# Kernel optimization log

Measured on AMD Instinct MI355X. Metric: run time of the kernel, lower is better.

## Reference

```python
import jax, jax.numpy as jnp
import numpy as np

MARGIN = 0.3
POS_THRESH_M = 25.0
NEG_THRESH_M = 100.0
EARTH_R = 6371000.0
B, D = 1024, 256


def _pairwise_haversine(gps):
    # gps: [B,2] degrees -> [B,B] meters
    lat = jnp.deg2rad(gps[:, 0])
    dlat = jnp.deg2rad(gps[None, :, 0] - gps[:, None, 0])
    dlon = jnp.deg2rad(gps[None, :, 1] - gps[:, None, 1])
    a = jnp.sin(dlat / 2) ** 2 + jnp.cos(lat)[:, None] * jnp.cos(lat)[None, :] * jnp.sin(dlon / 2) ** 2
    return EARTH_R * 2.0 * jnp.arctan2(jnp.sqrt(a), jnp.sqrt(1.0 - a))


def _pairwise_euclidean(emb):
    # faithful to torch.norm(emb[None]-emb[:,None], dim=-1), with safe sqrt at 0
    diff = emb[None, :, :] - emb[:, None, :]          # [B,B,D]
    sq = jnp.sum(diff * diff, axis=-1)                # [B,B]
    return jnp.where(sq > 0, jnp.sqrt(jnp.where(sq > 0, sq, 1.0)), 0.0)


def setup_inputs() -> dict:
    key = jax.random.key(0)
    k1, k2 = jax.random.split(key)
    embeddings = jax.random.normal(k1, (B, D), dtype=jnp.float32)
    # small geographic box (~222 m x ~182 m) so both positive (<25 m) and
    # negative (>100 m) pairs exist for nearly every anchor
    base = jnp.array([35.0, 139.0], dtype=jnp.float32)
    gps_coords = base + jax.random.uniform(k2, (B, 2), dtype=jnp.float32) * 0.002
    return {"embeddings": embeddings, "gps_coords": gps_coords}


def reference(embeddings, gps_coords):
    n = embeddings.shape[0]
    gps_d = _pairwise_haversine(gps_coords)           # [B,B]
    emb_d = _pairwise_euclidean(embeddings)           # [B,B]
    eye = jnp.eye(n, dtype=bool)
    pos_mask = (gps_d < POS_THRESH_M) & ~eye
    neg_mask = gps_d > NEG_THRESH_M

    has_pos = jnp.any(pos_mask, axis=1)
    has_neg = jnp.any(neg_mask, axis=1)
    valid = has_pos & has_neg                         # anchors contributing a triplet

    # hardest positive per anchor (masked max)
    d_ap = jnp.max(jnp.where(pos_mask, emb_d, -1.0), axis=1)          # [B]

    # semi-hard negatives: d_ap < d < d_ap + margin among negatives
    semi_mask = neg_mask & (emb_d > d_ap[:, None]) & (emb_d < d_ap[:, None] + MARGIN)
    has_semi = jnp.any(semi_mask, axis=1)
    BIG = jnp.float32(1e9)
    semi_min = jnp.min(jnp.where(semi_mask, emb_d, BIG), axis=1)
    neg_min = jnp.min(jnp.where(neg_mask, emb_d, BIG), axis=1)        # fallback: hardest negative
    d_an = jnp.where(has_semi, semi_min, neg_min)

    triplet = jax.nn.relu(d_ap - d_an + MARGIN)
    triplet = jnp.where(valid, triplet, 0.0)
    n_triplets = jnp.sum(valid.astype(jnp.float32))
    loss = jnp.sum(triplet) / jnp.maximum(n_triplets, 1.0)
    return loss
```

## Files before the change

kernel.cpp:

```cpp
#include <hip/hip_runtime.h>
#include <hip/hip_bf16.h>

typedef __attribute__((ext_vector_type(8))) short bf16x8;
typedef __attribute__((ext_vector_type(4))) float f32x4;

#define NB 1024
#define ND 256
#define KC 512
#define MARGINF 0.3f
#define BIGV 1e9f
#define D2R 0.017453292519943295f
#define HD2R 0.008726646259971648f

#define A_POS 3.8495040e-12f
#define A_NEG 6.1592064e-11f

__device__ __forceinline__ float d4(float4 a, float4 b, float acc) {
    return fmaf(a.x,b.x, fmaf(a.y,b.y, fmaf(a.z,b.z, fmaf(a.w,b.w, acc))));
}

__global__ __launch_bounds__(256) void prep_kernel(
    const float* __restrict__ emb, const float* __restrict__ gps,
    float4* __restrict__ prep, unsigned short* __restrict__ C)
{
    const int tid = threadIdx.x;
    const int row = blockIdx.x*16 + (tid >> 4);
    const int kk  = tid & 15;
    const float4* r4 = (const float4*)emb + (size_t)row*64;
    float s = 0.f;
    #pragma unroll
    for (int c = 0; c < 4; ++c) {
        float4 v = r4[kk + 16*c];
        s = d4(v, v, s);
        float fv[4] = {v.x, v.y, v.z, v.w};
        unsigned short hh[4], ll[4];
        #pragma unroll
        for (int q = 0; q < 4; ++q) {
            __hip_bfloat16 hb = __float2bfloat16(fv[q]);
            float hf = __bfloat162float(hb);
            __hip_bfloat16 lb = __float2bfloat16(fv[q] - hf);
            hh[q] = *(unsigned short*)&hb;
            ll[q] = *(unsigned short*)&lb;
        }
        *(ushort4*)(C + (size_t)row*KC +       4*(kk+16*c)) = make_ushort4(hh[0],hh[1],hh[2],hh[3]);
        *(ushort4*)(C + (size_t)row*KC + 256 + 4*(kk+16*c)) = make_ushort4(ll[0],ll[1],ll[2],ll[3]);
    }
    #pragma unroll
    for (int off = 1; off < 16; off <<= 1) s += __shfl_xor(s, off);
    if (kk == 0) {
        float2 g = ((const float2*)gps)[row];
        prep[row] = make_float4(s, g.x, g.y, cosf(g.x * D2R));
    }
}

__global__ __launch_bounds__(256) void gram_mfma(
    const unsigned short* __restrict__ C, const float4* __restrict__ prep,
    float* __restrict__ sEnc, float* __restrict__ pP)
{
    __shared__ float sRed[64][33];

    const int tid = threadIdx.x, lane = tid & 63, w = tid >> 6;
    const int wr = w >> 1, wc = w & 1;
    const int ib = blockIdx.x & 15, jb = blockIdx.x >> 4;
    const int i0 = ib*64, j0 = jb*64;
    const int lr = lane & 15, lk = lane >> 4;
    const short* Cs = (const short*)C;

    f32x4 acc[2][2] = {};
    #pragma unroll 4
    for (int ks = 0; ks < 16; ++ks) {
        bf16x8 a0 = *(const bf16x8*)(Cs + (size_t)(i0 + wr*32      + lr)*KC + ks*32 + lk*8);
        bf16x8 a1 = *(const bf16x8*)(Cs + (size_t)(i0 + wr*32 + 16 + lr)*KC + ks*32 + lk*8);
        bf16x8 b0 = *(const bf16x8*)(Cs + (size_t)(j0 + wc*32      + lr)*KC + ks*32 + lk*8);
        bf16x8 b1 = *(const bf16x8*)(Cs + (size_t)(j0 + wc*32 + 16 + lr)*KC + ks*32 + lk*8);
        acc[0][0] = __builtin_amdgcn_mfma_f32_16x16x32_bf16(a0, b0, acc[0][0], 0, 0, 0);
        acc[0][1] = __builtin_amdgcn_mfma_f32_16x16x32_bf16(a0, b1, acc[0][1], 0, 0, 0);
        acc[1][0] = __builtin_amdgcn_mfma_f32_16x16x32_bf16(a1, b0, acc[1][0], 0, 0, 0);
        acc[1][1] = __builtin_amdgcn_mfma_f32_16x16x32_bf16(a1, b1, acc[1][1], 0, 0, 0);
    }

    float4 pj[2];
    pj[0] = prep[j0 + wc*32 + lr];
    pj[1] = prep[j0 + wc*32 + 16 + lr];

    #pragma unroll
    for (int fi = 0; fi < 2; ++fi) {
        #pragma unroll
        for (int r = 0; r < 4; ++r) {
            const int rl = wr*32 + fi*16 + lk*4 + r;
            const int gi = i0 + rl;
            const float4 pi = prep[gi];
            float pmax = -1.f;
            #pragma unroll
            for (int fj = 0; fj < 2; ++fj) {
                const int gj = j0 + wc*32 + fj*16 + lr;
                float d2v = pi.x + pj[fj].x - 2.f*acc[fi][fj][r];
                d2v = d2v > 0.f ? d2v : 0.f;
                const float sla = sinf((pj[fj].y - pi.y) * HD2R);
                const float slo = sinf((pj[fj].z - pi.z) * HD2R);
                const float hav = fmaf(sla, sla, (pi.w * pj[fj].w) * (slo*slo));
                const bool pos = (hav < A_POS) && (gi != gj);
                const bool neg = (hav > A_NEG);
                pmax = fmaxf(pmax, pos ? d2v : -1.f);
                sEnc[(size_t)gi*NB + gj] = neg ? d2v : BIGV;
            }
            sRed[rl][lr + 16*wc] = pmax;
        }
    }
    __syncthreads();
    if (tid < 64) {
        float m = sRed[tid][0];
        #pragma unroll
        for (int c = 1; c < 32; ++c) m = fmaxf(m, sRed[tid][c]);
        pP[(i0 + tid)*16 + jb] = m;
    }
}

__global__ __launch_bounds__(256) void rows_kernel(
    const float* __restrict__ sEnc, const float* __restrict__ pP,
    float* __restrict__ tri, float* __restrict__ val)
{
    const int tid = threadIdx.x, lane = tid & 63, w = tid >> 6;
    const int i = blockIdx.x*4 + w;

    float p = pP[i*16 + (lane & 15)];
    #pragma unroll
    for (int off = 1; off < 16; off <<= 1) p = fmaxf(p, __shfl_xor(p, off));
    const float dap2 = p;
    const bool has_pos = dap2 > -0.5f;
    float lo2 = -1.f, hi2 = -1.f;
    if (has_pos) { const float hb = sqrtf(dap2) + MARGINF; lo2 = dap2; hi2 = hb*hb; }

    float nmin = BIGV, smin = BIGV;
    const float4* __restrict__ row = (const float4*)sEnc + (size_t)i*256;
    #pragma unroll
    for (int pss = 0; pss < 4; ++pss) {
        const float4 x = row[pss*64 + lane];
        #pragma unroll
        for (int q = 0; q < 4; ++q) {
            const float xc = (q==0) ? x.x : (q==1) ? x.y : (q==2) ? x.z : x.w;
            nmin = fminf(nmin, xc);
            smin = fminf(smin, (xc > lo2 && xc < hi2) ? xc : BIGV);
        }
    }
    #pragma unroll
    for (int off = 1; off < 64; off <<= 1) {
        nmin = fminf(nmin, __shfl_xor(nmin, off));
        smin = fminf(smin, __shfl_xor(smin, off));
    }
    if (lane == 0) {
        const bool has_neg  = nmin < 0.5f*BIGV;
        const bool has_semi = smin < 0.5f*BIGV;
        const float dan2 = has_semi ? smin : nmin;
        const float dap  = has_pos ? sqrtf(dap2) : 0.f;
        float t = dap - sqrtf(dan2) + MARGINF;
        t = t > 0.f ? t : 0.f;
        const bool valid = has_pos && has_neg;
        tri[i] = valid ? t : 0.f;
        val[i] = valid ? 1.f : 0.f;
    }
}

__global__ __launch_bounds__(256) void finalize_kernel(
    const float* __restrict__ tri, const float* __restrict__ val, float* __restrict__ out)
{
    const int tid = threadIdx.x;
    float st = 0.f, sv = 0.f;
    #pragma unroll
    for (int g = 0; g < 4; ++g) { st += tri[tid + (g<<8)]; sv += val[tid + (g<<8)]; }
    #pragma unroll
    for (int off = 1; off < 64; off <<= 1) { st += __shfl_xor(st, off); sv += __shfl_xor(sv, off); }
    __shared__ float rt[4], rv[4];
    if ((tid & 63) == 0) { rt[tid>>6] = st; rv[tid>>6] = sv; }
    __syncthreads();
    if (tid == 0) {
        float t = rt[0]+rt[1]+rt[2]+rt[3];
        float v = rv[0]+rv[1]+rv[2]+rv[3];
        out[0] = t / fmaxf(v, 1.f);
    }
}

extern "C" void kernel_launch(void* const* d_in, const int* in_sizes, int n_in,
                              void* d_out, int out_size, void* d_ws, size_t ws_size,
                              hipStream_t stream) {
    const float* emb = (const float*)d_in[0];
    const float* gps = (const float*)d_in[1];
    float* ws = (float*)d_ws;

    float*          sEnc = ws;
    unsigned short* Cbf  = (unsigned short*)(ws + 1048576);
    float4*         prep = (float4*)(ws + 1048576 + 262144);
    float*          pP   = ws + 1048576 + 262144 + 4096;
    float*          tri  = pP + 16384;
    float*          val  = tri + 1024;

    prep_kernel<<<64, 256, 0, stream>>>(emb, gps, prep, Cbf);
    gram_mfma<<<256, 256, 0, stream>>>(Cbf, prep, sEnc, pP);
    rows_kernel<<<256, 256, 0, stream>>>(sEnc, pP, tri, val);
    finalize_kernel<<<1, 256, 0, stream>>>(tri, val, (float*)d_out);
}
```

Measured before the change: 28.58 us.

## Fuse prep kernel into gram MFMA with on-the-fly bf16 hi/lo split

Removes the separate prep kernel and computes row norms, gps cosines and the bf16 high/low split inside the gram kernel, with norms and gps staged in shared memory. The MFMA loop now does three products per k-chunk (HH, LH, HL), where the old code ran a single product over a concatenated hi|lo layout. This saves one launch and the round trip through the intermediate bf16 buffer. In exchange every block redoes the conversion and norm work for its tiles, reads fp32 rows directly, and issues more MFMAs.

Measured after the change: 27.42 us. -4.1%, faster.

```diff
diff --git a/kernel.cpp b/kernel.cpp
--- a/kernel.cpp
+++ b/kernel.cpp
@@ -6,7 +6,6 @@
 
 #define NB 1024
 #define ND 256
-#define KC 512
 #define MARGINF 0.3f
 #define BIGV 1e9f
 #define D2R 0.017453292519943295f
@@ -19,69 +18,82 @@
     return fmaf(a.x,b.x, fmaf(a.y,b.y, fmaf(a.z,b.z, fmaf(a.w,b.w, acc))));
 }
 
-__global__ __launch_bounds__(256) void prep_kernel(
+__device__ __forceinline__ void splitHL(float4 v0, float4 v1, bf16x8& H, bf16x8& L) {
+    float f[8] = {v0.x, v0.y, v0.z, v0.w, v1.x, v1.y, v1.z, v1.w};
+    #pragma unroll
+    for (int q = 0; q < 8; ++q) {
+        __hip_bfloat16 h = __float2bfloat16(f[q]);
+        float hf = __bfloat162float(h);
+        __hip_bfloat16 l = __float2bfloat16(f[q] - hf);
+        H[q] = *(short*)&h;
+        L[q] = *(short*)&l;
+    }
+}
+
+__global__ __launch_bounds__(256) void gram_mfma(
     const float* __restrict__ emb, const float* __restrict__ gps,
-    float4* __restrict__ prep, unsigned short* __restrict__ C)
-{
-    const int tid = threadIdx.x;
-    const int row = blockIdx.x*16 + (tid >> 4);
-    const int kk  = tid & 15;
-    const float4* r4 = (const float4*)emb + (size_t)row*64;
-    float s = 0.f;
-    #pragma unroll
-    for (int c = 0; c < 4; ++c) {
-        float4 v = r4[kk + 16*c];
-        s = d4(v, v, s);
-        float fv[4] = {v.x, v.y, v.z, v.w};
-        unsigned short hh[4], ll[4];
-        #pragma unroll
-        for (int q = 0; q < 4; ++q) {
-            __hip_bfloat16 hb = __float2bfloat16(fv[q]);
-            float hf = __bfloat162float(hb);
-            __hip_bfloat16 lb = __float2bfloat16(fv[q] - hf);
-            hh[q] = *(unsigned short*)&hb;
-            ll[q] = *(unsigned short*)&lb;
-        }
-        *(ushort4*)(C + (size_t)row*KC +       4*(kk+16*c)) = make_ushort4(hh[0],hh[1],hh[2],hh[3]);
-        *(ushort4*)(C + (size_t)row*KC + 256 + 4*(kk+16*c)) = make_ushort4(ll[0],ll[1],ll[2],ll[3]);
-    }
-    #pragma unroll
-    for (int off = 1; off < 16; off <<= 1) s += __shfl_xor(s, off);
-    if (kk == 0) {
-        float2 g = ((const float2*)gps)[row];
-        prep[row] = make_float4(s, g.x, g.y, cosf(g.x * D2R));
-    }
-}
-
-__global__ __launch_bounds__(256) void gram_mfma(
-    const unsigned short* __restrict__ C, const float4* __restrict__ prep,
     float* __restrict__ sEnc, float* __restrict__ pP)
 {
-    __shared__ float sRed[64][33];
+    __shared__ float  sSqI[64], sSqJ[64];
+    __shared__ float4 sGI[64], sGJ[64];
+    __shared__ float  sRed[64][33];
 
     const int tid = threadIdx.x, lane = tid & 63, w = tid >> 6;
     const int wr = w >> 1, wc = w & 1;
     const int ib = blockIdx.x & 15, jb = blockIdx.x >> 4;
     const int i0 = ib*64, j0 = jb*64;
     const int lr = lane & 15, lk = lane >> 4;
-    const short* Cs = (const short*)C;
+    const float4* __restrict__ emb4 = (const float4*)emb;
+
+    {
+        const int half = tid & 1, r = (tid >> 1) & 63;
+        const int base = (tid < 128) ? i0 : j0;
+        const float4* rp = emb4 + (size_t)(base + r)*64 + half*32;
+        float s = 0.f;
+        #pragma unroll
+        for (int q = 0; q < 32; ++q) s = d4(rp[q], rp[q], s);
+        s += __shfl_xor(s, 1);
+        if (half == 0) { if (tid < 128) sSqI[r] = s; else sSqJ[r] = s; }
+    }
+    if (tid < 128) {
+        const int r = tid & 63;
+        const int base = (tid < 64) ? i0 : j0;
+        float2 g = ((const float2*)gps)[base + r];
+        float4 gi = make_float4(g.x, g.y, cosf(g.x * D2R), 0.f);
+        if (tid < 64) sGI[r] = gi; else sGJ[r] = gi;
+    }
+    __syncthreads();
 
     f32x4 acc[2][2] = {};
-    #pragma unroll 4
-    for (int ks = 0; ks < 16; ++ks) {
-        bf16x8 a0 = *(const bf16x8*)(Cs + (size_t)(i0 + wr*32      + lr)*KC + ks*32 + lk*8);
-        bf16x8 a1 = *(const bf16x8*)(Cs + (size_t)(i0 + wr*32 + 16 + lr)*KC + ks*32 + lk*8);
-        bf16x8 b0 = *(const bf16x8*)(Cs + (size_t)(j0 + wc*32      + lr)*KC + ks*32 + lk*8);
-        bf16x8 b1 = *(const bf16x8*)(Cs + (size_t)(j0 + wc*32 + 16 + lr)*KC + ks*32 + lk*8);
-        acc[0][0] = __builtin_amdgcn_mfma_f32_16x16x32_bf16(a0, b0, acc[0][0], 0, 0, 0);
-        acc[0][1] = __builtin_amdgcn_mfma_f32_16x16x32_bf16(a0, b1, acc[0][1], 0, 0, 0);
-        acc[1][0] = __builtin_amdgcn_mfma_f32_16x16x32_bf16(a1, b0, acc[1][0], 0, 0, 0);
-        acc[1][1] = __builtin_amdgcn_mfma_f32_16x16x32_bf16(a1, b1, acc[1][1], 0, 0, 0);
-    }
-
-    float4 pj[2];
-    pj[0] = prep[j0 + wc*32 + lr];
-    pj[1] = prep[j0 + wc*32 + 16 + lr];
+    #pragma unroll 2
+    for (int k8 = 0; k8 < 8; ++k8) {
+        const int co = k8*8 + lk*2;
+        const float4* pa0 = emb4 + (size_t)(i0 + wr*32      + lr)*64 + co;
+        const float4* pa1 = emb4 + (size_t)(i0 + wr*32 + 16 + lr)*64 + co;
+        const float4* pb0 = emb4 + (size_t)(j0 + wc*32      + lr)*64 + co;
+        const float4* pb1 = emb4 + (size_t)(j0 + wc*32 + 16 + lr)*64 + co;
+        bf16x8 a0H,a0L,a1H,a1L,b0H,b0L,b1H,b1L;
+        splitHL(pa0[0], pa0[1], a0H, a0L);
+        splitHL(pa1[0], pa1[1], a1H, a1L);
+        splitHL(pb0[0], pb0[1], b0H, b0L);
+        splitHL(pb1[0], pb1[1], b1H, b1L);
+        acc[0][0] = __builtin_amdgcn_mfma_f32_16x16x32_bf16(a0H, b0H, acc[0][0], 0,0,0);
+        acc[0][1] = __builtin_amdgcn_mfma_f32_16x16x32_bf16(a0H, b1H, acc[0][1], 0,0,0);
+        acc[1][0] = __builtin_amdgcn_mfma_f32_16x16x32_bf16(a1H, b0H, acc[1][0], 0,0,0);
+        acc[1][1] = __builtin_amdgcn_mfma_f32_16x16x32_bf16(a1H, b1H, acc[1][1], 0,0,0);
+        acc[0][0] = __builtin_amdgcn_mfma_f32_16x16x32_bf16(a0L, b0H, acc[0][0], 0,0,0);
+        acc[0][1] = __builtin_amdgcn_mfma_f32_16x16x32_bf16(a0L, b1H, acc[0][1], 0,0,0);
+        acc[1][0] = __builtin_amdgcn_mfma_f32_16x16x32_bf16(a1L, b0H, acc[1][0], 0,0,0);
+        acc[1][1] = __builtin_amdgcn_mfma_f32_16x16x32_bf16(a1L, b1H, acc[1][1], 0,0,0);
+        acc[0][0] = __builtin_amdgcn_mfma_f32_16x16x32_bf16(a0H, b0L, acc[0][0], 0,0,0);
+        acc[0][1] = __builtin_amdgcn_mfma_f32_16x16x32_bf16(a0H, b1L, acc[0][1], 0,0,0);
+        acc[1][0] = __builtin_amdgcn_mfma_f32_16x16x32_bf16(a1H, b0L, acc[1][0], 0,0,0);
+        acc[1][1] = __builtin_amdgcn_mfma_f32_16x16x32_bf16(a1H, b1L, acc[1][1], 0,0,0);
+    }
+
+    float sqj[2]; float4 gj2[2];
+    sqj[0] = sSqJ[wc*32 + lr];      gj2[0] = sGJ[wc*32 + lr];
+    sqj[1] = sSqJ[wc*32 + 16 + lr]; gj2[1] = sGJ[wc*32 + 16 + lr];
 
     #pragma unroll
     for (int fi = 0; fi < 2; ++fi) {
@@ -89,16 +101,17 @@
         for (int r = 0; r < 4; ++r) {
             const int rl = wr*32 + fi*16 + lk*4 + r;
             const int gi = i0 + rl;
-            const float4 pi = prep[gi];
+            const float sqi = sSqI[rl];
+            const float4 gvi = sGI[rl];
             float pmax = -1.f;
             #pragma unroll
             for (int fj = 0; fj < 2; ++fj) {
                 const int gj = j0 + wc*32 + fj*16 + lr;
-                float d2v = pi.x + pj[fj].x - 2.f*acc[fi][fj][r];
+                float d2v = sqi + sqj[fj] - 2.f*acc[fi][fj][r];
                 d2v = d2v > 0.f ? d2v : 0.f;
-                const float sla = sinf((pj[fj].y - pi.y) * HD2R);
-                const float slo = sinf((pj[fj].z - pi.z) * HD2R);
-                const float hav = fmaf(sla, sla, (pi.w * pj[fj].w) * (slo*slo));
+                const float sla = sinf((gj2[fj].x - gvi.x) * HD2R);
+                const float slo = sinf((gj2[fj].y - gvi.y) * HD2R);
+                const float hav = fmaf(sla, sla, (gvi.z * gj2[fj].z) * (slo*slo));
                 const bool pos = (hav < A_POS) && (gi != gj);
                 const bool neg = (hav > A_NEG);
                 pmax = fmaxf(pmax, pos ? d2v : -1.f);
@@ -187,15 +200,12 @@
     const float* gps = (const float*)d_in[1];
     float* ws = (float*)d_ws;
 
-    float*          sEnc = ws;
-    unsigned short* Cbf  = (unsigned short*)(ws + 1048576);
-    float4*         prep = (float4*)(ws + 1048576 + 262144);
-    float*          pP   = ws + 1048576 + 262144 + 4096;
-    float*          tri  = pP + 16384;
-    float*          val  = tri + 1024;
-
-    prep_kernel<<<64, 256, 0, stream>>>(emb, gps, prep, Cbf);
-    gram_mfma<<<256, 256, 0, stream>>>(Cbf, prep, sEnc, pP);
+    float* sEnc = ws;
+    float* pP   = ws + 1048576;
+    float* tri  = pP + 16384;
+    float* val  = tri + 1024;
+
+    gram_mfma<<<256, 256, 0, stream>>>(emb, gps, sEnc, pP);
     rows_kernel<<<256, 256, 0, stream>>>(sEnc, pP, tri, val);
     finalize_kernel<<<1, 256, 0, stream>>>(tri, val, (float*)d_out);
 }
```
